# Performance work log

Hardware: AMD Instinct MI355X
Metric: run time of the kernel (lower is better)

Reference implementation:

```python
import jax, jax.numpy as jnp
import numpy as np

N, M, D = 8192, 8192, 256

def setup_inputs() -> dict:
    key = jax.random.key(0)
    kx, ky = jax.random.split(key)
    x = jax.random.normal(kx, (N, D), dtype=jnp.float32)
    y = jax.random.normal(ky, (M, D), dtype=jnp.float32)
    gamma = jnp.float32(1.0)  # learnable scalar parameter
    return {"x": x, "y": y, "gamma": gamma}

def reference(x, y, gamma):
    # Flatten trailing dims (matches x.view(x.size(0), -1))
    x = x.reshape(x.shape[0], -1)
    y = y.reshape(y.shape[0], -1)
    x_sq = jnp.sum(x * x, axis=-1)  # [N]
    y_sq = jnp.sum(y * y, axis=-1)  # [M]
    xy = x @ y.T                    # [N, M]
    sqdist = jnp.maximum(x_sq[:, None] + y_sq[None, :] - 2.0 * xy, 0.0)
    return jnp.exp(-gamma * sqdist)
```

## Files before the change

### kernel.cpp

```cpp
#include <hip/hip_runtime.h>
#include <stdint.h>


typedef __attribute__((ext_vector_type(4))) float f32x4;

#define NN 8192
#define MM 8192
#define DD 256
#define BK 64

__global__ __launch_bounds__(256) void prep_kernel(
    const float* __restrict__ x, const float* __restrict__ y,
    unsigned char* __restrict__ xb, unsigned char* __restrict__ yb,
    float* __restrict__ xsq, float* __restrict__ ysq) {
  const int lane = threadIdx.x & 63;
  const int row  = blockIdx.x * 4 + (threadIdx.x >> 6);

  const float* src = x;
  unsigned char* dst = xb;
  float* sq = xsq;
  int r = row;
  if (row >= NN) { src = y; dst = yb; sq = ysq; r = row - NN; }

  const float4 v = reinterpret_cast<const float4*>(src + (size_t)r * DD)[lane];
  float s = v.x * v.x + v.y * v.y + v.z * v.z + v.w * v.w;

  int w = 0;
  w = __builtin_amdgcn_cvt_pk_fp8_f32(v.x, v.y, w, false);
  w = __builtin_amdgcn_cvt_pk_fp8_f32(v.z, v.w, w, true);
  reinterpret_cast<int*>(dst + (size_t)r * DD)[lane] = w;

  #pragma unroll
  for (int o = 32; o > 0; o >>= 1) s += __shfl_down(s, o);
  if (lane == 0) sq[r] = s;
}

__global__ __launch_bounds__(256, 2) void rbf_gemm_kernel(
    const unsigned char* __restrict__ xb, const unsigned char* __restrict__ yb,
    const float* __restrict__ xsq, const float* __restrict__ ysq,
    const float* __restrict__ gamma, float* __restrict__ out) {
  __shared__ unsigned char As[128 * BK];
  __shared__ unsigned char Bs[128 * BK];

  const int tid   = threadIdx.x;
  const int lane  = tid & 63;
  const int wave  = tid >> 6;
  const int waveM = wave >> 1;
  const int waveN = wave & 1;
  const int row0  = blockIdx.y * 128;
  const int col0  = blockIdx.x * 128;

  f32x4 acc[4][4] = {};

  const int crow = lane >> 2;
  const int sseg = ((lane & 3) ^ (crow & 3)) * 16;

  const int fm = lane & 15;
  const int g  = lane >> 4;

  for (int kk = 0; kk < DD; kk += BK) {
    __syncthreads();
    #pragma unroll
    for (int q = 0; q < 2; ++q) {
      const int c = wave * 2 + q;
      const unsigned char* ga =
          xb + (size_t)(row0 + c * 16 + crow) * DD + kk + sseg;
      __builtin_amdgcn_global_load_lds(
          (const __attribute__((address_space(1))) void*)ga,
          (__attribute__((address_space(3))) void*)(As + c * 1024), 16, 0, 0);
      const unsigned char* gb =
          yb + (size_t)(col0 + c * 16 + crow) * DD + kk + sseg;
      __builtin_amdgcn_global_load_lds(
          (const __attribute__((address_space(1))) void*)gb,
          (__attribute__((address_space(3))) void*)(Bs + c * 1024), 16, 0, 0);
    }
    __syncthreads();

    #pragma unroll
    for (int h = 0; h < 2; ++h) {
      const int s = h * 2 + (g >> 1);
      const int foff = fm * 64 + ((s ^ (fm & 3)) * 16) + (g & 1) * 8;
      long a[4], b[4];
      #pragma unroll
      for (int i = 0; i < 4; ++i)
        a[i] = *reinterpret_cast<const long*>(
            As + (waveM * 4 + i) * 1024 + foff);
      #pragma unroll
      for (int j = 0; j < 4; ++j)
        b[j] = *reinterpret_cast<const long*>(
            Bs + (waveN * 4 + j) * 1024 + foff);

      #pragma unroll
      for (int i = 0; i < 4; ++i)
        #pragma unroll
        for (int j = 0; j < 4; ++j)
          acc[i][j] = __builtin_amdgcn_mfma_f32_16x16x32_fp8_fp8(
              a[i], b[j], acc[i][j], 0, 0, 0);
    }
  }

  const float gm = gamma[0];
  const int colb = col0 + waveN * 64 + (lane & 15);
  float ysv[4];
  #pragma unroll
  for (int j = 0; j < 4; ++j) ysv[j] = ysq[colb + j * 16];

  #pragma unroll
  for (int i = 0; i < 4; ++i) {
    #pragma unroll
    for (int r = 0; r < 4; ++r) {
      const int row = row0 + waveM * 64 + i * 16 + (lane >> 4) * 4 + r;
      const float xsv = xsq[row];
      #pragma unroll
      for (int j = 0; j < 4; ++j) {
        float s = xsv + ysv[j] - 2.0f * acc[i][j][r];
        s = fmaxf(s, 0.0f);
        out[(size_t)row * MM + colb + j * 16] = __expf(-gm * s);
      }
    }
  }
}

extern "C" void kernel_launch(void* const* d_in, const int* in_sizes, int n_in,
                              void* d_out, int out_size, void* d_ws, size_t ws_size,
                              hipStream_t stream) {
  const float* x     = (const float*)d_in[0];
  const float* y     = (const float*)d_in[1];
  const float* gamma = (const float*)d_in[2];
  float* out = (float*)d_out;

  unsigned char* xb = (unsigned char*)d_ws;
  unsigned char* yb = xb + (size_t)NN * DD;
  float* xsq = (float*)(yb + (size_t)MM * DD);
  float* ysq = xsq + NN;

  prep_kernel<<<(NN + MM) / 4, 256, 0, stream>>>(x, y, xb, yb, xsq, ysq);

  dim3 grid(MM / 128, NN / 128);
  rbf_gemm_kernel<<<grid, 256, 0, stream>>>(xb, yb, xsq, ysq, gamma, out);
}
```

Measured before the change: 285.9 us.

## Use K=128 scaled FP8 MFMA with wider LDS tiles and nontemporal output stores

After: 287.1 us. About the same (+0.4%).

```diff
diff --git a/kernel.cpp b/kernel.cpp
--- a/kernel.cpp
+++ b/kernel.cpp
@@ -3,11 +3,12 @@
 
 
 typedef __attribute__((ext_vector_type(4))) float f32x4;
+typedef __attribute__((ext_vector_type(8))) int   i32x8;
 
 #define NN 8192
 #define MM 8192
 #define DD 256
-#define BK 64
+#define BK 128
 
 __global__ __launch_bounds__(256) void prep_kernel(
     const float* __restrict__ x, const float* __restrict__ y,
@@ -52,51 +53,64 @@
 
   f32x4 acc[4][4] = {};
 
-  const int crow = lane >> 2;
-  const int sseg = ((lane & 3) ^ (crow & 3)) * 16;
+  const int srow = lane >> 3;
+  const int sseg = ((lane & 7) ^ (lane >> 3)) * 16;
 
   const int fm = lane & 15;
   const int g  = lane >> 4;
+  const int off_lo = fm * 128 + (((2 * g)     ^ (fm & 7)) * 16);
+  const int off_hi = fm * 128 + (((2 * g + 1) ^ (fm & 7)) * 16);
 
-  for (int kk = 0; kk < DD; kk += BK) {
+  #pragma unroll
+  for (int kt = 0; kt < 2; ++kt) {
+    const int kk = kt * BK;
     __syncthreads();
     #pragma unroll
     for (int q = 0; q < 2; ++q) {
       const int c = wave * 2 + q;
-      const unsigned char* ga =
-          xb + (size_t)(row0 + c * 16 + crow) * DD + kk + sseg;
-      __builtin_amdgcn_global_load_lds(
-          (const __attribute__((address_space(1))) void*)ga,
-          (__attribute__((address_space(3))) void*)(As + c * 1024), 16, 0, 0);
-      const unsigned char* gb =
-          yb + (size_t)(col0 + c * 16 + crow) * DD + kk + sseg;
-      __builtin_amdgcn_global_load_lds(
-          (const __attribute__((address_space(1))) void*)gb,
-          (__attribute__((address_space(3))) void*)(Bs + c * 1024), 16, 0, 0);
+      #pragma unroll
+      for (int p = 0; p < 2; ++p) {
+        const unsigned char* ga =
+            xb + (size_t)(row0 + c * 16 + p * 8 + srow) * DD + kk + sseg;
+        __builtin_amdgcn_global_load_lds(
+            (const __attribute__((address_space(1))) void*)ga,
+            (__attribute__((address_space(3))) void*)(As + c * 2048 + p * 1024),
+            16, 0, 0);
+        const unsigned char* gb =
+            yb + (size_t)(col0 + c * 16 + p * 8 + srow) * DD + kk + sseg;
+        __builtin_amdgcn_global_load_lds(
+            (const __attribute__((address_space(1))) void*)gb,
+            (__attribute__((address_space(3))) void*)(Bs + c * 2048 + p * 1024),
+            16, 0, 0);
+      }
     }
     __syncthreads();
 
+    i32x8 a[4], b[4];
     #pragma unroll
-    for (int h = 0; h < 2; ++h) {
-      const int s = h * 2 + (g >> 1);
-      const int foff = fm * 64 + ((s ^ (fm & 3)) * 16) + (g & 1) * 8;
-      long a[4], b[4];
-      #pragma unroll
-      for (int i = 0; i < 4; ++i)
-        a[i] = *reinterpret_cast<const long*>(
-            As + (waveM * 4 + i) * 1024 + foff);
+    for (int i = 0; i < 4; ++i) {
+      const unsigned char* base = As + (waveM * 4 + i) * 2048;
+      const int4 lo = *reinterpret_cast<const int4*>(base + off_lo);
+      const int4 hi = *reinterpret_cast<const int4*>(base + off_hi);
+      a[i][0] = lo.x; a[i][1] = lo.y; a[i][2] = lo.z; a[i][3] = lo.w;
+      a[i][4] = hi.x; a[i][5] = hi.y; a[i][6] = hi.z; a[i][7] = hi.w;
+    }
+    #pragma unroll
+    for (int j = 0; j < 4; ++j) {
+      const unsigned char* base = Bs + (waveN * 4 + j) * 2048;
+      const int4 lo = *reinterpret_cast<const int4*>(base + off_lo);
+      const int4 hi = *reinterpret_cast<const int4*>(base + off_hi);
+      b[j][0] = lo.x; b[j][1] = lo.y; b[j][2] = lo.z; b[j][3] = lo.w;
+      b[j][4] = hi.x; b[j][5] = hi.y; b[j][6] = hi.z; b[j][7] = hi.w;
+    }
+
+    #pragma unroll
+    for (int i = 0; i < 4; ++i)
       #pragma unroll
       for (int j = 0; j < 4; ++j)
-        b[j] = *reinterpret_cast<const long*>(
-            Bs + (waveN * 4 + j) * 1024 + foff);
-
-      #pragma unroll
-      for (int i = 0; i < 4; ++i)
-        #pragma unroll
-        for (int j = 0; j < 4; ++j)
-          acc[i][j] = __builtin_amdgcn_mfma_f32_16x16x32_fp8_fp8(
-              a[i], b[j], acc[i][j], 0, 0, 0);
-    }
+        acc[i][j] = __builtin_amdgcn_mfma_scale_f32_16x16x128_f8f6f4(
+            a[i], b[j], acc[i][j], 0, 0,
+            0, 0x7F7F7F7F, 0, 0x7F7F7F7F);
   }
 
   const float gm = gamma[0];
@@ -115,7 +129,8 @@
       for (int j = 0; j < 4; ++j) {
         float s = xsv + ysv[j] - 2.0f * acc[i][j][r];
         s = fmaxf(s, 0.0f);
-        out[(size_t)row * MM + colb + j * 16] = __expf(-gm * s);
+        __builtin_nontemporal_store(__expf(-gm * s),
+                                    out + (size_t)row * MM + colb + j * 16);
       }
     }
   }
```
